# Optimization experiments

Measured on AMD Instinct MI355X. Metric: run time of the kernel, lower is better.

## Reference

```python
import jax, jax.numpy as jnp
import numpy as np

EMBED_DIM = 768
NUM_HEADS = 12


def setup_inputs() -> dict:
    key = jax.random.key(0)
    ks = jax.random.split(key, 9)
    B, N, C = 16, 1024, EMBED_DIM
    std = 1.0 / np.sqrt(C)
    x = jax.random.normal(ks[0], (B, N, C), dtype=jnp.float32)
    def w(k):
        return jax.random.normal(k, (C, C), dtype=jnp.float32) * std
    def b(k):
        return jax.random.normal(k, (C,), dtype=jnp.float32) * 0.01
    return {
        "x": x,
        "Wq": w(ks[1]), "bq": b(ks[2]),
        "Wk": w(ks[3]), "bk": b(ks[4]),
        "Wv": w(ks[5]), "bv": b(ks[6]),
        "Wo": w(ks[7]), "bo": b(ks[8]),
    }


def reference(x, Wq, bq, Wk, bk, Wv, bv, Wo, bo):
    B, N, C = x.shape
    H = NUM_HEADS
    Dh = C // H
    scale = 1.0 / np.sqrt(Dh)

    q = x @ Wq + bq  # (B, N, C)
    k = x @ Wk + bk
    v = x @ Wv + bv

    # Faithful to the original: (B, N, H, Dh) -> reshape(B*H, N, Dh)
    # WITHOUT transposing, exactly as torch_mla_core does (row-major reshape).
    q2 = q.reshape(B * H, N, Dh)
    k2 = k.reshape(B * H, N, Dh)
    v2 = v.reshape(B * H, N, Dh)

    scores = jnp.einsum('gld,gmd->glm', q2, k2) * scale  # (B*H, N, N)
    attn = jax.nn.softmax(scores, axis=-1)
    ctx2 = jnp.einsum('glm,gmd->gld', attn, v2)  # (B*H, N, Dh)

    ctx = ctx2.reshape(B, H, N, Dh).transpose(0, 2, 1, 3).reshape(B, N, C)
    out = ctx @ Wo + bo
    return out
```

## Files before the change

### kernel.cpp

```cpp
#include <hip/hip_runtime.h>
#include <cstdint>
#include <cstddef>

typedef unsigned short u16;
typedef __attribute__((ext_vector_type(8))) short s8v;
typedef __attribute__((ext_vector_type(4))) float f4v;
typedef __attribute__((ext_vector_type(8))) u16 u16x8;

#define AS1 __attribute__((address_space(1)))
#define AS3 __attribute__((address_space(3)))

#define BATCH 16
#define SEQ   1024
#define EMBED 768
#define HEADS 12
#define DH    64
#define GROUPS (BATCH*HEADS)
#define MTOT  (BATCH*SEQ)

__device__ __forceinline__ u16 f2bf(float f) {
    union { float f; uint32_t u; } v; v.f = f;
    uint32_t r = v.u + 0x7fffu + ((v.u >> 16) & 1u);
    return (u16)(r >> 16);
}

__device__ __forceinline__ void gll16(const u16* g, u16* l) {
    __builtin_amdgcn_global_load_lds((AS1 void*)g, (AS3 void*)l, 16, 0, 0);
}

__global__ void k_pack_x(const float* __restrict__ x, u16* __restrict__ xb, int n) {
    int i = (blockIdx.x * 256 + threadIdx.x) * 4;
    if (i + 3 < n) {
        float4 f = *(const float4*)(x + i);
        ushort4 o;
        o.x = f2bf(f.x); o.y = f2bf(f.y); o.z = f2bf(f.z); o.w = f2bf(f.w);
        *(ushort4*)(xb + i) = o;
    }
}

__global__ void k_pack_w(const float* __restrict__ Wq, const float* __restrict__ Wk,
                         const float* __restrict__ Wv, const float* __restrict__ Wo,
                         const float* __restrict__ bq, const float* __restrict__ bk,
                         const float* __restrict__ bv,
                         u16* __restrict__ wqkvT, u16* __restrict__ woT,
                         float* __restrict__ bqkv)
{
    const int NQKV = 2304 * 768;
    const int NO = 768 * 768;
    int t = blockIdx.x * 256 + threadIdx.x;
    if (t < NQKV) {
        int n = t % 2304, k = t / 2304;
        const float* src; int nn; float sc;
        if (n < 768)       { src = Wq; nn = n;        sc = 0.125f; }
        else if (n < 1536) { src = Wk; nn = n - 768;  sc = 1.0f;   }
        else               { src = Wv; nn = n - 1536; sc = 1.0f;   }
        wqkvT[(size_t)n * 768 + k] = f2bf(src[(size_t)k * 768 + nn] * sc);
    } else if (t < NQKV + NO) {
        int t2 = t - NQKV;
        int n = t2 % 768, k = t2 / 768;
        woT[(size_t)n * 768 + k] = f2bf(Wo[(size_t)k * 768 + n]);
    } else if (t < NQKV + NO + 2304) {
        int t3 = t - NQKV - NO;
        bqkv[t3] = (t3 < 768) ? bq[t3] * 0.125f
                 : ((t3 < 1536) ? bk[t3 - 768] : bv[t3 - 1536]);
    }
}

template<int MODE>
__global__ __launch_bounds__(256) void k_gemm(
    const u16* __restrict__ A, const u16* __restrict__ BT,
    const float* __restrict__ bias,
    u16* __restrict__ oq, u16* __restrict__ okk, u16* __restrict__ ov,
    float* __restrict__ of)
{
    __shared__ __attribute__((aligned(16))) u16 As[128 * 32];
    __shared__ __attribute__((aligned(16))) u16 Bs[128 * 32];
    const int tid = threadIdx.x;
    const int m0 = blockIdx.x * 128;
    const int n0 = blockIdx.y * 128;
    const int wv = tid >> 6;
    const int ln = tid & 63;
    const int l15 = ln & 15, quad = ln >> 4;
    const int wm = (wv >> 1) * 64, wn = (wv & 1) * 64;
    const int r = tid >> 2, c8 = (tid & 3) * 8;

    const u16* gA0 = A + (size_t)(m0 + r) * 768 + c8;
    const u16* gA1 = gA0 + 64 * 768;
    const u16* gB0 = BT + (size_t)(n0 + r) * 768 + c8;
    const u16* gB1 = gB0 + 64 * 768;
    u16* lA0 = As + wv * 512;
    u16* lA1 = As + 2048 + wv * 512;
    u16* lB0 = Bs + wv * 512;
    u16* lB1 = Bs + 2048 + wv * 512;

    f4v acc[4][4] = {};

    for (int kt = 0; kt < 24; ++kt) {
        const int ko = kt * 32;
        gll16(gA0 + ko, lA0);
        gll16(gA1 + ko, lA1);
        gll16(gB0 + ko, lB0);
        gll16(gB1 + ko, lB1);
        __syncthreads();
        s8v aF[4], bF[4];
#pragma unroll
        for (int i = 0; i < 4; ++i)
            aF[i] = *(const s8v*)(As + (wm + i * 16 + l15) * 32 + quad * 8);
#pragma unroll
        for (int j = 0; j < 4; ++j)
            bF[j] = *(const s8v*)(Bs + (wn + j * 16 + l15) * 32 + quad * 8);
#pragma unroll
        for (int i = 0; i < 4; ++i)
#pragma unroll
            for (int j = 0; j < 4; ++j)
                acc[i][j] = __builtin_amdgcn_mfma_f32_16x16x32_bf16(aF[i], bF[j], acc[i][j], 0, 0, 0);
        __syncthreads();
    }

#pragma unroll
    for (int j = 0; j < 4; ++j) {
        int n = n0 + wn + j * 16 + l15;
        float bs = bias[n];
        if (MODE == 0) {
            u16* dst; int nn;
            if (n < 768)       { dst = oq;  nn = n; }
            else if (n < 1536) { dst = okk; nn = n - 768; }
            else               { dst = ov;  nn = n - 1536; }
#pragma unroll
            for (int i = 0; i < 4; ++i) {
                int mrow = m0 + wm + i * 16 + quad * 4;
#pragma unroll
                for (int rg = 0; rg < 4; ++rg)
                    dst[(size_t)(mrow + rg) * 768 + nn] = f2bf(acc[i][j][rg] + bs);
            }
        } else {
#pragma unroll
            for (int i = 0; i < 4; ++i) {
                int mrow = m0 + wm + i * 16 + quad * 4;
#pragma unroll
                for (int rg = 0; rg < 4; ++rg)
                    of[(size_t)(mrow + rg) * 768 + n] = acc[i][j][rg] + bs;
            }
        }
    }
}

__global__ void k_transpose_v(const u16* __restrict__ v, u16* __restrict__ vt) {
    __shared__ __attribute__((aligned(16))) u16 ts[64 * 72];
    int g = blockIdx.x >> 4;
    int l0 = (blockIdx.x & 15) << 6;
    const u16* vg = v + (size_t)g * 65536;
    u16* vtg = vt + (size_t)g * 65536;
    int tid = threadIdx.x;
#pragma unroll
    for (int c = tid; c < 512; c += 256) {
        int l = c >> 3, d0 = (c & 7) * 8;
        *(uint4*)(ts + l * 72 + d0) = *(const uint4*)(vg + (size_t)(l0 + l) * 64 + d0);
    }
    __syncthreads();
#pragma unroll
    for (int c = tid; c < 512; c += 256) {
        int d = c >> 3, lc = (c & 7) * 8;
        u16x8 tv;
#pragma unroll
        for (int i = 0; i < 8; ++i) tv[i] = ts[(lc + i) * 72 + d];
        *(u16x8*)(vtg + (size_t)d * 1024 + l0 + lc) = tv;
    }
}

#define PS_OFF(q_, c_) ( ((q_) << 7) + ((((((c_) >> 3) ^ ((((q_) >> 2) & 3) << 1)) & 15) << 3) | ((c_) & 7)) )
#define KS_OFF(r_, c_) ( ((r_) >> 3) * 544 + ((r_) & 7) * 64 + (c_) )

__global__ __launch_bounds__(256) void k_attn(
    const u16* __restrict__ qb, const u16* __restrict__ kb,
    const u16* __restrict__ vt, u16* __restrict__ ctx)
{
    __shared__ __attribute__((aligned(16))) u16 Ks[16 * 544];
    __shared__ __attribute__((aligned(16))) u16 Vts[64 * 136];
    __shared__ __attribute__((aligned(16))) u16 U[64 * 128];

    const int g = blockIdx.x >> 4;
    const int q0 = (blockIdx.x & 15) << 6;
    const int tid = threadIdx.x, wv = tid >> 6;
    const int ln = tid & 63, l15 = ln & 15, quad = ln >> 4;
    const u16* qg = qb + (size_t)g * 65536;
    const u16* kg = kb + (size_t)g * 65536;
    const u16* vtg = vt + (size_t)g * 65536;

#pragma unroll
    for (int c = tid; c < 512; c += 256) {
        int r = c >> 3, d0 = (c & 7) * 8;
        *(uint4*)(U + r * 72 + d0) = *(const uint4*)(qg + (size_t)(q0 + r) * 64 + d0);
    }
    __syncthreads();
    s8v aQ0 = *(const s8v*)(U + (wv * 16 + l15) * 72 + quad * 8);
    s8v aQ1 = *(const s8v*)(U + (wv * 16 + l15) * 72 + 32 + quad * 8);

    f4v o[4] = {};
    float rsum[4] = {0.f, 0.f, 0.f, 0.f};

    for (int jt = 0; jt < 8; ++jt) {
        const int n0 = jt * 128;
        __syncthreads();

#pragma unroll
        for (int i = 0; i < 4; ++i) {
            int g8 = wv * 4 + i;
            gll16(kg + (size_t)(n0 + g8 * 8) * 64 + ln * 8, Ks + g8 * 544);
        }
#pragma unroll
        for (int c = tid; c < 1024; c += 256) {
            int d = c >> 4, c0 = (c & 15) * 8;
            *(uint4*)(Vts + d * 136 + c0) = *(const uint4*)(vtg + (size_t)d * 1024 + n0 + c0);
        }
        __syncthreads();

        f4v s[8];
#pragma unroll
        for (int ns = 0; ns < 8; ++ns) {
            int rK = ns * 16 + l15;
            s8v b0 = *(const s8v*)(Ks + KS_OFF(rK, quad * 8));
            s8v b1 = *(const s8v*)(Ks + KS_OFF(rK, quad * 8 + 32));
            f4v t = {};
            t = __builtin_amdgcn_mfma_f32_16x16x32_bf16(aQ0, b0, t, 0, 0, 0);
            t = __builtin_amdgcn_mfma_f32_16x16x32_bf16(aQ1, b1, t, 0, 0, 0);
            s[ns] = t;
        }

#pragma unroll
        for (int ns = 0; ns < 8; ++ns)
#pragma unroll
            for (int rg = 0; rg < 4; ++rg) {
                float p = __expf(s[ns][rg]);
                s[ns][rg] = p;
                rsum[rg] += p;
            }

#pragma unroll
        for (int ns = 0; ns < 8; ++ns)
#pragma unroll
            for (int rg = 0; rg < 4; ++rg) {
                int q = wv * 16 + quad * 4 + rg;
                U[PS_OFF(q, ns * 16 + l15)] = f2bf(s[ns][rg]);
            }

#pragma unroll
        for (int ks = 0; ks < 4; ++ks) {
            int m = wv * 16 + l15;
            int blk = ks * 4 + quad;
            int sw = ((l15 >> 2) & 3) << 1;
            s8v aP = *(const s8v*)(U + (m << 7) + (((blk ^ sw) & 15) << 3));
#pragma unroll
            for (int ds = 0; ds < 4; ++ds) {
                s8v bV = *(const s8v*)(Vts + (ds * 16 + l15) * 136 + ks * 32 + quad * 8);
                o[ds] = __builtin_amdgcn_mfma_f32_16x16x32_bf16(aP, bV, o[ds], 0, 0, 0);
            }
        }
    }

#pragma unroll
    for (int rg = 0; rg < 4; ++rg) {
        float v = rsum[rg];
        v += __shfl_xor(v, 1, 64);
        v += __shfl_xor(v, 2, 64);
        v += __shfl_xor(v, 4, 64);
        v += __shfl_xor(v, 8, 64);
        rsum[rg] = v;
    }

    const int b = g / 12, h = g % 12;
    u16* cbase = ctx + (size_t)b * 1024 * 768 + h * 64;
#pragma unroll
    for (int rg = 0; rg < 4; ++rg) {
        float inv = 1.0f / rsum[rg];
        int row = q0 + wv * 16 + quad * 4 + rg;
#pragma unroll
        for (int ds = 0; ds < 4; ++ds)
            cbase[(size_t)row * 768 + ds * 16 + l15] = f2bf(o[ds][rg] * inv);
    }
}

extern "C" void kernel_launch(void* const* d_in, const int* in_sizes, int n_in,
                              void* d_out, int out_size, void* d_ws, size_t ws_size,
                              hipStream_t stream) {
    const float* x  = (const float*)d_in[0];
    const float* Wq = (const float*)d_in[1];
    const float* bq = (const float*)d_in[2];
    const float* Wk = (const float*)d_in[3];
    const float* bk = (const float*)d_in[4];
    const float* Wv = (const float*)d_in[5];
    const float* bv = (const float*)d_in[6];
    const float* Wo = (const float*)d_in[7];
    const float* bo = (const float*)d_in[8];
    float* out = (float*)d_out;

    const size_t NTOK = (size_t)MTOT * EMBED;
    char* w = (char*)d_ws;
    u16* xb    = (u16*)w;              w += NTOK * 2;
    u16* qb    = (u16*)w;              w += NTOK * 2;
    u16* kb    = (u16*)w;              w += NTOK * 2;
    u16* vb    = (u16*)w;              w += NTOK * 2;
    u16* vtb   = (u16*)w;              w += NTOK * 2;
    u16* wqkvT = (u16*)w;              w += (size_t)2304 * 768 * 2;
    u16* woT   = (u16*)w;              w += (size_t)768 * 768 * 2;
    float* bqkv = (float*)w;           w += 2304 * 4;
    u16* ctx = xb;

    k_pack_x<<<12288, 256, 0, stream>>>(x, xb, (int)NTOK);
    k_pack_w<<<9225, 256, 0, stream>>>(Wq, Wk, Wv, Wo, bq, bk, bv, wqkvT, woT, bqkv);

    dim3 g1(128, 18);
    k_gemm<0><<<g1, 256, 0, stream>>>(xb, wqkvT, bqkv, qb, kb, vb, nullptr);

    k_transpose_v<<<3072, 256, 0, stream>>>(vb, vtb);
    k_attn<<<3072, 256, 0, stream>>>(qb, kb, vtb, ctx);

    dim3 g2(128, 6);
    k_gemm<1><<<g2, 256, 0, stream>>>(ctx, woT, bo, nullptr, nullptr, nullptr, out);
}
```

Before: 368.5 us.

## Retile attention to 128-query blocks with 32x32 MFMA and XOR-swizzled LDS

Rewrites the attention kernel so each block handles 128 queries, with 32 per wave, over 64-key tiles, using the 32x32x16 bf16 MFMA instead of 16x16x32. K, V^T, Q and the P tile share one XOR-swizzle layout in LDS, and the async global-to-LDS K load is replaced by plain vector copies. Occupancy is hinted at 4 blocks per CU, and half as many blocks are launched. The larger query tile means K/V are reloaded half as often, at the cost of more loop iterations, more accumulator registers, and scalar 16-bit stores of P into LDS.

```diff
diff --git a/kernel.cpp b/kernel.cpp
--- a/kernel.cpp
+++ b/kernel.cpp
@@ -1,10 +1,12 @@
 #include <hip/hip_runtime.h>
+#include <hip/hip_bf16.h>
 #include <cstdint>
 #include <cstddef>
 
 typedef unsigned short u16;
 typedef __attribute__((ext_vector_type(8))) short s8v;
 typedef __attribute__((ext_vector_type(4))) float f4v;
+typedef __attribute__((ext_vector_type(16))) float f16v;
 typedef __attribute__((ext_vector_type(8))) u16 u16x8;
 
 #define AS1 __attribute__((address_space(1)))
@@ -15,13 +17,18 @@
 #define EMBED 768
 #define HEADS 12
 #define DH    64
-#define GROUPS (BATCH*HEADS)
 #define MTOT  (BATCH*SEQ)
 
 __device__ __forceinline__ u16 f2bf(float f) {
     union { float f; uint32_t u; } v; v.f = f;
     uint32_t r = v.u + 0x7fffu + ((v.u >> 16) & 1u);
     return (u16)(r >> 16);
+}
+
+__device__ __forceinline__ unsigned pk2bf(float a, float b) {
+    union { __hip_bfloat162 h; unsigned u; } cv;
+    cv.h = __float22bfloat162_rn(make_float2(a, b));
+    return cv.u;
 }
 
 __device__ __forceinline__ void gll16(const u16* g, u16* l) {
@@ -168,115 +175,106 @@
     }
 }
 
-#define PS_OFF(q_, c_) ( ((q_) << 7) + ((((((c_) >> 3) ^ ((((q_) >> 2) & 3) << 1)) & 15) << 3) | ((c_) & 7)) )
-#define KS_OFF(r_, c_) ( ((r_) >> 3) * 544 + ((r_) & 7) * 64 + (c_) )
-
-__global__ __launch_bounds__(256) void k_attn(
+#define SW(r_, c_) ( ((r_) << 6) + (((((c_) >> 3) ^ ((r_) & 7)) & 7) << 3) + ((c_) & 7) )
+
+__global__ __launch_bounds__(256, 4) void k_attn(
     const u16* __restrict__ qb, const u16* __restrict__ kb,
     const u16* __restrict__ vt, u16* __restrict__ ctx)
 {
-    __shared__ __attribute__((aligned(16))) u16 Ks[16 * 544];
-    __shared__ __attribute__((aligned(16))) u16 Vts[64 * 136];
-    __shared__ __attribute__((aligned(16))) u16 U[64 * 128];
-
-    const int g = blockIdx.x >> 4;
-    const int q0 = (blockIdx.x & 15) << 6;
-    const int tid = threadIdx.x, wv = tid >> 6;
-    const int ln = tid & 63, l15 = ln & 15, quad = ln >> 4;
+    __shared__ __attribute__((aligned(16))) u16 Ks[64 * 64];
+    __shared__ __attribute__((aligned(16))) u16 Vts[64 * 64];
+    __shared__ __attribute__((aligned(16))) u16 U[128 * 64];
+
+    const int g = blockIdx.x >> 3;
+    const int q0 = (blockIdx.x & 7) << 7;
+    const int tid = threadIdx.x, wv = tid >> 6, ln = tid & 63;
+    const int l31 = ln & 31, hf = ln >> 5;
     const u16* qg = qb + (size_t)g * 65536;
     const u16* kg = kb + (size_t)g * 65536;
     const u16* vtg = vt + (size_t)g * 65536;
 
 #pragma unroll
-    for (int c = tid; c < 512; c += 256) {
-        int r = c >> 3, d0 = (c & 7) * 8;
-        *(uint4*)(U + r * 72 + d0) = *(const uint4*)(qg + (size_t)(q0 + r) * 64 + d0);
+    for (int i = 0; i < 4; ++i) {
+        int t = tid + i * 256;
+        int r = t >> 3, cb = (t & 7) << 3;
+        *(uint4*)(U + SW(r, cb)) = *(const uint4*)(qg + (size_t)(q0 + r) * 64 + cb);
     }
     __syncthreads();
-    s8v aQ0 = *(const s8v*)(U + (wv * 16 + l15) * 72 + quad * 8);
-    s8v aQ1 = *(const s8v*)(U + (wv * 16 + l15) * 72 + 32 + quad * 8);
-
-    f4v o[4] = {};
-    float rsum[4] = {0.f, 0.f, 0.f, 0.f};
-
-    for (int jt = 0; jt < 8; ++jt) {
-        const int n0 = jt * 128;
+    s8v aQ[4];
+#pragma unroll
+    for (int kb2 = 0; kb2 < 4; ++kb2)
+        aQ[kb2] = *(const s8v*)(U + SW(wv * 32 + l31, kb2 * 16 + hf * 8));
+
+    f16v o0 = {}, o1 = {};
+    float rsum[16];
+#pragma unroll
+    for (int i = 0; i < 16; ++i) rsum[i] = 0.f;
+
+    for (int jt = 0; jt < 16; ++jt) {
+        const int n0 = jt * 64;
         __syncthreads();
-
-#pragma unroll
-        for (int i = 0; i < 4; ++i) {
-            int g8 = wv * 4 + i;
-            gll16(kg + (size_t)(n0 + g8 * 8) * 64 + ln * 8, Ks + g8 * 544);
-        }
-#pragma unroll
-        for (int c = tid; c < 1024; c += 256) {
-            int d = c >> 4, c0 = (c & 15) * 8;
-            *(uint4*)(Vts + d * 136 + c0) = *(const uint4*)(vtg + (size_t)d * 1024 + n0 + c0);
+#pragma unroll
+        for (int i = 0; i < 2; ++i) {
+            int t = tid + i * 256;
+            int r = t >> 3, cb = (t & 7) << 3;
+            *(uint4*)(Ks + SW(r, cb))  = *(const uint4*)(kg + (size_t)(n0 + r) * 64 + cb);
+            *(uint4*)(Vts + SW(r, cb)) = *(const uint4*)(vtg + (size_t)r * 1024 + n0 + cb);
         }
         __syncthreads();
 
-        f4v s[8];
-#pragma unroll
-        for (int ns = 0; ns < 8; ++ns) {
-            int rK = ns * 16 + l15;
-            s8v b0 = *(const s8v*)(Ks + KS_OFF(rK, quad * 8));
-            s8v b1 = *(const s8v*)(Ks + KS_OFF(rK, quad * 8 + 32));
-            f4v t = {};
-            t = __builtin_amdgcn_mfma_f32_16x16x32_bf16(aQ0, b0, t, 0, 0, 0);
-            t = __builtin_amdgcn_mfma_f32_16x16x32_bf16(aQ1, b1, t, 0, 0, 0);
-            s[ns] = t;
-        }
-
-#pragma unroll
-        for (int ns = 0; ns < 8; ++ns)
-#pragma unroll
-            for (int rg = 0; rg < 4; ++rg) {
-                float p = __expf(s[ns][rg]);
-                s[ns][rg] = p;
-                rsum[rg] += p;
+#pragma unroll
+        for (int nb = 0; nb < 2; ++nb) {
+            f16v s = {};
+#pragma unroll
+            for (int kb2 = 0; kb2 < 4; ++kb2) {
+                s8v bK = *(const s8v*)(Ks + SW(nb * 32 + l31, kb2 * 16 + hf * 8));
+                s = __builtin_amdgcn_mfma_f32_32x32x16_bf16(aQ[kb2], bK, s, 0, 0, 0);
             }
-
-#pragma unroll
-        for (int ns = 0; ns < 8; ++ns)
-#pragma unroll
-            for (int rg = 0; rg < 4; ++rg) {
-                int q = wv * 16 + quad * 4 + rg;
-                U[PS_OFF(q, ns * 16 + l15)] = f2bf(s[ns][rg]);
+            int col = nb * 32 + l31;
+#pragma unroll
+            for (int reg = 0; reg < 16; reg += 2) {
+                float p0 = __expf(s[reg]), p1 = __expf(s[reg + 1]);
+                rsum[reg] += p0; rsum[reg + 1] += p1;
+                unsigned u = pk2bf(p0, p1);
+                int row = wv * 32 + (reg & 3) + ((reg >> 2) << 3) + (hf << 2);
+                U[SW(row, col)] = (u16)u;
+                U[SW(row + 1, col)] = (u16)(u >> 16);
             }
-
-#pragma unroll
-        for (int ks = 0; ks < 4; ++ks) {
-            int m = wv * 16 + l15;
-            int blk = ks * 4 + quad;
-            int sw = ((l15 >> 2) & 3) << 1;
-            s8v aP = *(const s8v*)(U + (m << 7) + (((blk ^ sw) & 15) << 3));
-#pragma unroll
-            for (int ds = 0; ds < 4; ++ds) {
-                s8v bV = *(const s8v*)(Vts + (ds * 16 + l15) * 136 + ks * 32 + quad * 8);
-                o[ds] = __builtin_amdgcn_mfma_f32_16x16x32_bf16(aP, bV, o[ds], 0, 0, 0);
-            }
-        }
-    }
-
-#pragma unroll
-    for (int rg = 0; rg < 4; ++rg) {
-        float v = rsum[rg];
+        }
+
+#pragma unroll
+        for (int kb2 = 0; kb2 < 4; ++kb2) {
+            int co = kb2 * 16 + hf * 8;
+            s8v aP = *(const s8v*)(U + SW(wv * 32 + l31, co));
+            s8v bV0 = *(const s8v*)(Vts + SW(l31, co));
+            s8v bV1 = *(const s8v*)(Vts + SW(32 + l31, co));
+            o0 = __builtin_amdgcn_mfma_f32_32x32x16_bf16(aP, bV0, o0, 0, 0, 0);
+            o1 = __builtin_amdgcn_mfma_f32_32x32x16_bf16(aP, bV1, o1, 0, 0, 0);
+        }
+    }
+
+#pragma unroll
+    for (int reg = 0; reg < 16; ++reg) {
+        float v = rsum[reg];
         v += __shfl_xor(v, 1, 64);
         v += __shfl_xor(v, 2, 64);
         v += __shfl_xor(v, 4, 64);
         v += __shfl_xor(v, 8, 64);
-        rsum[rg] = v;
-    }
-
-    const int b = g / 12, h = g % 12;
-    u16* cbase = ctx + (size_t)b * 1024 * 768 + h * 64;
-#pragma unroll
-    for (int rg = 0; rg < 4; ++rg) {
-        float inv = 1.0f / rsum[rg];
-        int row = q0 + wv * 16 + quad * 4 + rg;
-#pragma unroll
-        for (int ds = 0; ds < 4; ++ds)
-            cbase[(size_t)row * 768 + ds * 16 + l15] = f2bf(o[ds][rg] * inv);
+        v += __shfl_xor(v, 16, 64);
+        rsum[reg] = 1.0f / v;
+    }
+
+    const int b = g / 12, hd = g % 12;
+    u16* cbase = ctx + (size_t)b * 786432 + hd * 64;
+#pragma unroll
+    for (int nb = 0; nb < 2; ++nb) {
+        int d = nb * 32 + l31;
+        const f16v& ov = nb ? o1 : o0;
+#pragma unroll
+        for (int reg = 0; reg < 16; ++reg) {
+            int q = q0 + wv * 32 + (reg & 3) + ((reg >> 2) << 3) + (hf << 2);
+            cbase[(size_t)q * 768 + d] = f2bf(ov[reg] * rsum[reg]);
+        }
     }
 }
 
@@ -313,7 +311,7 @@
     k_gemm<0><<<g1, 256, 0, stream>>>(xb, wqkvT, bqkv, qb, kb, vb, nullptr);
 
     k_transpose_v<<<3072, 256, 0, stream>>>(vb, vtb);
-    k_attn<<<3072, 256, 0, stream>>>(qb, kb, vtb, ctx);
+    k_attn<<<1536, 256, 0, stream>>>(qb, kb, vtb, ctx);
 
     dim3 g2(128, 6);
     k_gemm<1><<<g2, 256, 0, stream>>>(ctx, woT, bo, nullptr, nullptr, nullptr, out);
```

After: 436.0 us. +18.3%, slower.
